# Kernel tuning notes

Measured on AMD Instinct MI355X. Metric: run time of the kernel, lower is better.

The kernel has to match this reference:

```python
import jax, jax.numpy as jnp
import numpy as np

CT1, CT2, ETA = 0.15, 0.1, 0.5
B, K, C = 65536, 50, 10


def setup_inputs() -> dict:
    key = jax.random.key(0)
    ks = jax.random.split(key, 8)
    # xavier_normal-ish scales for the small learned params
    att = jax.random.normal(ks[5], (C,), jnp.float32) * (np.sqrt(2.0) * np.sqrt(2.0 / (C + 1)))
    proj = jax.random.normal(ks[6], (C, C), jnp.float32) * (np.sqrt(2.0) * np.sqrt(2.0 / (C + C)))
    return {
        "anchors_weak": jax.random.normal(ks[0], (B, C), jnp.float32),
        "anchors_strong": jax.random.normal(ks[1], (B, C), jnp.float32),
        "anchors": jax.random.normal(ks[2], (B, C), jnp.float32),
        "neighbors": jax.random.normal(ks[3], (B, K, C), jnp.float32),
        "labels": jax.random.randint(ks[4], (B,), 0, C),
        "index": jnp.arange(B),
        "att": att,
        "proj_param": proj,
    }


def reference(anchors_weak, anchors_strong, anchors, neighbors, labels, index, att, proj_param):
    # confidence mask on weak-augmentation probabilities
    wap = jax.nn.softmax(anchors_weak, axis=1)              # [B,C]
    mask0 = jnp.max(wap, axis=1) > CT1
    idx0 = jnp.nonzero(mask0)[0]                            # data-dependent (eager)

    wap = wap[idx0]                                         # [b,C]
    nbp = jax.nn.softmax(neighbors, axis=2)[idx0]           # [b,K,C]
    ap = jax.nn.softmax(anchors, axis=1)[idx0]              # [b,C]
    a_strong = anchors_strong[idx0]                         # [b,C]
    img_f = anchors[idx0]                                   # [b,C]
    nb_f = neighbors[idx0]                                  # [b,K,C]
    b, c = wap.shape

    # einsum('kk,ijk->ijk', P, X) multiplies by diag(P)
    d = jnp.diagonal(proj_param)                            # [C]
    zi = img_f[:, None, :] * d                              # [b,K,C] (broadcast expand)
    zj = nb_f * d                                           # [b,K,C]
    zizj = zi * zj                                          # cross_product attention
    att_score = jax.nn.leaky_relu(jnp.einsum('k,bjk->bj', att, zizj))  # [b,K]
    att_val = jax.nn.softmax(att_score, axis=1)[..., None]  # [b,K,1]
    q_hat = jnp.sum(att_val * nbp, axis=1)                  # [b,C]

    beta = jnp.sum((ap - q_hat) ** 2, axis=1)               # [b] = ||.||^2
    k = max(int(ETA * b), 1)
    topk_min = -jax.lax.top_k(-beta, k)[0]                  # k smallest
    tau = topk_min[-1] / jnp.exp(jnp.asarray(-1.0))
    alpha = -jnp.log(beta / tau)                            # [b]

    qi = wap ** alpha[:, None]
    qi = qi / jnp.sum(qi, axis=1, keepdims=True)
    q = jnp.where((alpha > 1.0)[:, None], qi, wap)          # [b,C]

    max_prob = jnp.max(q, axis=1)
    target = jnp.argmax(q, axis=1)
    mask = max_prob > CT2
    idx1 = jnp.nonzero(mask)[0]
    target_masked = target[idx1]
    n = int(idx1.shape[0])

    # class balancing (torch.unique equivalent via fixed-size counts)
    counts = jax.ops.segment_sum(jnp.ones_like(target_masked, dtype=jnp.float32),
                                 target_masked, num_segments=c)
    freq = counts / n
    weight = jnp.where(counts > 0, 1.0 / jnp.log(1.02 + freq), 1.0)  # [C]

    inp = a_strong[idx1]                                    # [n,C]
    input_prob = jax.nn.log_softmax(inp, axis=1)
    q_mask = q[idx1]                                        # [n,C]
    w_avg = weight[None, :] / jnp.sum(weight) * jnp.mean(weight)
    loss = -jnp.sum(w_avg * q_mask * input_prob) / n

    return (loss, target_masked, labels[idx0][idx1], n)
```

## Files before the change

### kernel.cpp

```cpp
#include <hip/hip_runtime.h>
#include <math.h>

#define CC 10
#define KK 50

__global__ __launch_bounds__(256)
void kA(const float* __restrict__ aw, const float* __restrict__ an,
        const float* __restrict__ nbr, const float* __restrict__ att,
        const float* __restrict__ proj,
        float* __restrict__ wap, float* __restrict__ beta,
        int* __restrict__ flag0, int* __restrict__ hist, int B)
{
  int i = blockIdx.x * 256 + threadIdx.x;
  if (i >= B) return;

  float coef[CC];
#pragma unroll
  for (int c = 0; c < CC; ++c) { float d = proj[c * CC + c]; coef[c] = att[c] * d * d; }

  const float2* anp = reinterpret_cast<const float2*>(an + (size_t)i * CC);
  float av[CC];
#pragma unroll
  for (int c2 = 0; c2 < CC / 2; ++c2) { float2 t = anp[c2]; av[2*c2] = t.x; av[2*c2+1] = t.y; }
  float ci[CC];
#pragma unroll
  for (int c = 0; c < CC; ++c) ci[c] = coef[c] * av[c];

  const float2* rowp = reinterpret_cast<const float2*>(nbr + (size_t)i * (KK * CC));
  float den = 0.f;
  float qh[CC];
#pragma unroll
  for (int c = 0; c < CC; ++c) qh[c] = 0.f;

#pragma unroll 5
  for (int k = 0; k < KK; ++k) {
    float nb[CC];
#pragma unroll
    for (int c2 = 0; c2 < CC / 2; ++c2) {
      float2 t = rowp[k * (CC / 2) + c2];
      nb[2*c2] = t.x; nb[2*c2+1] = t.y;
    }
    float s = 0.f;
#pragma unroll
    for (int c = 0; c < CC; ++c) s = fmaf(ci[c], nb[c], s);
    s = (s > 0.f) ? s : 0.01f * s;
    float en[CC]; float sn = 0.f;
#pragma unroll
    for (int c = 0; c < CC; ++c) { en[c] = __expf(nb[c]); sn += en[c]; }
    float e = __expf(s);
    den += e;
    float esc = e * __builtin_amdgcn_rcpf(sn);
#pragma unroll
    for (int c = 0; c < CC; ++c) qh[c] = fmaf(esc, en[c], qh[c]);
  }
  float invd = __builtin_amdgcn_rcpf(den);

  float ap[CC]; float s2 = 0.f;
#pragma unroll
  for (int c = 0; c < CC; ++c) { ap[c] = __expf(av[c]); s2 += ap[c]; }
  float inv2 = __builtin_amdgcn_rcpf(s2);
  float dd = 0.f;
#pragma unroll
  for (int c = 0; c < CC; ++c) { float d1 = ap[c] * inv2 - qh[c] * invd; dd = fmaf(d1, d1, dd); }
  beta[i] = dd;

  const float2* awp = reinterpret_cast<const float2*>(aw + (size_t)i * CC);
  float wv[CC];
#pragma unroll
  for (int c2 = 0; c2 < CC / 2; ++c2) { float2 t = awp[c2]; wv[2*c2] = t.x; wv[2*c2+1] = t.y; }
  float ew[CC]; float sw = 0.f, mxw = 0.f;
#pragma unroll
  for (int c = 0; c < CC; ++c) { ew[c] = __expf(wv[c]); sw += ew[c]; mxw = fmaxf(mxw, ew[c]); }
  float rsw = __builtin_amdgcn_rcpf(sw);
  float2* wq = reinterpret_cast<float2*>(wap + (size_t)i * CC);
#pragma unroll
  for (int c2 = 0; c2 < CC / 2; ++c2) {
    float2 t; t.x = ew[2*c2] * rsw; t.y = ew[2*c2+1] * rsw; wq[c2] = t;
  }
  int f = (mxw * rsw > 0.15f) ? 1 : 0;
  flag0[i] = f;
  if (f) atomicAdd(&hist[__float_as_uint(dd) >> 16], 1);
}

__global__ __launch_bounds__(1024)
void k3b_sel(const int* __restrict__ hist, int* __restrict__ scal)
{
  __shared__ int tmp[1024];
  int t = threadIdx.x;
  int base = t * 64;
  const int4* h4 = reinterpret_cast<const int4*>(hist + base);
  int sum = 0;
#pragma unroll
  for (int jj = 0; jj < 16; ++jj) { int4 v = h4[jj]; sum += v.x + v.y + v.z + v.w; }
  tmp[t] = sum;
  __syncthreads();
  for (int off = 1; off < 1024; off <<= 1) {
    int v = (t >= off) ? tmp[t - off] : 0;
    __syncthreads();
    tmp[t] += v;
    __syncthreads();
  }
  int cumb = tmp[t] - sum;
  int b = tmp[1023];
  int k = (int)(0.5 * (double)b);
  if (k < 1) k = 1;
  if (t == 0) scal[4] = k;
  if (b > 0 && k > cumb && k <= cumb + sum) {
    int c = cumb;
    for (int jj = 0; jj < 64; ++jj) {
      int h = hist[base + jj];
      if (k <= c + h) { scal[2] = base + jj; scal[3] = k - c; break; }
      c += h;
    }
  }
  if (b == 0 && t == 0) { scal[2] = 0; scal[3] = 1; }
}

__global__ __launch_bounds__(256)
void k3c_hist2(const float* __restrict__ beta, const int* __restrict__ flag0,
               const int* __restrict__ scal, int* __restrict__ hist2, int B)
{
  int i = blockIdx.x * 256 + threadIdx.x;
  if (i >= B) return;
  if (flag0[i]) {
    unsigned key = __float_as_uint(beta[i]);
    if ((int)(key >> 16) == scal[2]) atomicAdd(&hist2[key & 0xFFFF], 1);
  }
}

__global__ __launch_bounds__(1024)
void k3d_tau(const int* __restrict__ hist2, int* __restrict__ scal,
             float* __restrict__ tau)
{
  __shared__ int tmp[1024];
  int t = threadIdx.x;
  int base = t * 64;
  const int4* h4 = reinterpret_cast<const int4*>(hist2 + base);
  int sum = 0;
#pragma unroll
  for (int jj = 0; jj < 16; ++jj) { int4 v = h4[jj]; sum += v.x + v.y + v.z + v.w; }
  tmp[t] = sum;
  __syncthreads();
  for (int off = 1; off < 1024; off <<= 1) {
    int v = (t >= off) ? tmp[t - off] : 0;
    __syncthreads();
    tmp[t] += v;
    __syncthreads();
  }
  int cumb = tmp[t] - sum;
  int k2 = scal[3];
  if (k2 > cumb && k2 <= cumb + sum) {
    int c = cumb;
    for (int jj = 0; jj < 64; ++jj) {
      int h = hist2[base + jj];
      if (k2 <= c + h) {
        unsigned key = (((unsigned)scal[2]) << 16) | (unsigned)(base + jj);
        float bk = __uint_as_float(key);
        *tau = bk / expf(-1.0f);
        break;
      }
      c += h;
    }
  }
}

__global__ __launch_bounds__(256)
void k4_q(const float* __restrict__ wap, const float* __restrict__ beta,
          const int* __restrict__ flag0, const float* __restrict__ tau_p,
          float* __restrict__ qbuf, int* __restrict__ target, int* __restrict__ flag1,
          int* __restrict__ counts, int* __restrict__ blockcnt, int B)
{
  __shared__ int lcnt[CC];
  if (threadIdx.x < CC) lcnt[threadIdx.x] = 0;
  __syncthreads();

  int i = blockIdx.x * 256 + threadIdx.x;
  int f = 0;
  if (i < B) {
    float tau = *tau_p;
    float w[CC];
    const float2* p = reinterpret_cast<const float2*>(wap + (size_t)i * CC);
#pragma unroll
    for (int c = 0; c < CC / 2; ++c) { float2 t = p[c]; w[2*c] = t.x; w[2*c+1] = t.y; }
    float alpha = -__logf(beta[i] / tau);
    float q[CC];
    if (alpha > 1.0f) {
      float s = 0.f;
#pragma unroll
      for (int c = 0; c < CC; ++c) { q[c] = __expf(alpha * __logf(w[c])); s += q[c]; }
#pragma unroll
      for (int c = 0; c < CC; ++c) q[c] = q[c] / s;
    } else {
#pragma unroll
      for (int c = 0; c < CC; ++c) q[c] = w[c];
    }
    float mp = q[0]; int tg = 0;
#pragma unroll
    for (int c = 1; c < CC; ++c) if (q[c] > mp) { mp = q[c]; tg = c; }
    f = (flag0[i] && (mp > 0.1f)) ? 1 : 0;
    float2* qo = reinterpret_cast<float2*>(qbuf + (size_t)i * CC);
#pragma unroll
    for (int c = 0; c < CC / 2; ++c) { float2 t; t.x = q[2*c]; t.y = q[2*c+1]; qo[c] = t; }
    target[i] = tg;
    flag1[i] = f;
    if (f) atomicAdd(&lcnt[tg], 1);
  }
  __shared__ int red[256];
  red[threadIdx.x] = f;
  __syncthreads();
  for (int off = 128; off; off >>= 1) {
    if (threadIdx.x < off) red[threadIdx.x] += red[threadIdx.x + off];
    __syncthreads();
  }
  if (threadIdx.x == 0) blockcnt[blockIdx.x] = red[0];
  if (threadIdx.x < CC) {
    int v = lcnt[threadIdx.x];
    if (v) atomicAdd(&counts[threadIdx.x], v);
  }
}

__global__ __launch_bounds__(256)
void k6_out(const int* __restrict__ flag1, const int* __restrict__ target,
            const int* __restrict__ labels, const int* __restrict__ blockcnt,
            const float* __restrict__ a_strong, const float* __restrict__ qbuf,
            const int* __restrict__ counts, float* __restrict__ out,
            float* __restrict__ lossp, int n_host, int nb, int B)
{
  __shared__ int tmp[256];
  __shared__ float wavg_s[CC];
  int t = threadIdx.x;

  int bv = (t < nb) ? blockcnt[t] : 0;
  tmp[t] = bv;
  __syncthreads();
  for (int off = 1; off < 256; off <<= 1) {
    int u = (t >= off) ? tmp[t - off] : 0;
    __syncthreads();
    tmp[t] += u;
    __syncthreads();
  }
  int n    = tmp[255];
  int boff = (blockIdx.x > 0) ? tmp[blockIdx.x - 1] : 0;
  if (t == 0) {
    float wt[CC]; float sumw = 0.f;
    for (int c = 0; c < CC; ++c) {
      int cnt = counts[c];
      float w_ = (cnt > 0) ? 1.0f / logf(1.02f + (float)cnt / (float)n) : 1.0f;
      wt[c] = w_; sumw += w_;
    }
    float meanw = sumw / (float)CC;
    for (int c = 0; c < CC; ++c) wavg_s[c] = wt[c] / sumw * meanw;
  }
  __syncthreads();

  int i = blockIdx.x * 256 + t;
  int f = (i < B) ? flag1[i] : 0;
  tmp[t] = f;
  __syncthreads();
  for (int off = 1; off < 256; off <<= 1) {
    int u = (t >= off) ? tmp[t - off] : 0;
    __syncthreads();
    tmp[t] += u;
    __syncthreads();
  }
  int pos = boff + tmp[t] - f;
  float part = 0.f;
  if (f) {
    out[1 + pos] = (float)target[i];
    out[1 + n_host + pos] = (float)labels[i];
    float x[CC];
    const float2* p = reinterpret_cast<const float2*>(a_strong + (size_t)i * CC);
#pragma unroll
    for (int c = 0; c < CC / 2; ++c) { float2 u2 = p[c]; x[2*c] = u2.x; x[2*c+1] = u2.y; }
    float m = x[0];
#pragma unroll
    for (int c = 1; c < CC; ++c) m = fmaxf(m, x[c]);
    float s = 0.f;
#pragma unroll
    for (int c = 0; c < CC; ++c) s += __expf(x[c] - m);
    float lse = m + __logf(s);
    const float2* qp = reinterpret_cast<const float2*>(qbuf + (size_t)i * CC);
    float q[CC];
#pragma unroll
    for (int c = 0; c < CC / 2; ++c) { float2 u2 = qp[c]; q[2*c] = u2.x; q[2*c+1] = u2.y; }
#pragma unroll
    for (int c = 0; c < CC; ++c) part += wavg_s[c] * q[c] * (x[c] - lse);
  }
  __shared__ float red[256];
  red[t] = part;
  __syncthreads();
  for (int off = 128; off; off >>= 1) {
    if (t < off) red[t] += red[t + off];
    __syncthreads();
  }
  if (t == 0) lossp[blockIdx.x] = red[0];
}

__global__ __launch_bounds__(256)
void k7_fin(const float* __restrict__ lossp, int nb, const int* __restrict__ blockcnt,
            float* __restrict__ out, int n_host)
{
  __shared__ float red[256];
  __shared__ int   redi[256];
  int t = threadIdx.x;
  float s = 0.f; int ns = 0;
  for (int jj = t; jj < nb; jj += 256) { s += lossp[jj]; ns += blockcnt[jj]; }
  red[t] = s; redi[t] = ns;
  __syncthreads();
  for (int off = 128; off; off >>= 1) {
    if (t < off) { red[t] += red[t + off]; redi[t] += redi[t + off]; }
    __syncthreads();
  }
  if (t == 0) {
    int n = redi[0];
    out[0] = -red[0] / (float)n;
    out[1 + 2 * n_host] = (float)n;
  }
}

extern "C" void kernel_launch(void* const* d_in, const int* in_sizes, int n_in,
                              void* d_out, int out_size, void* d_ws, size_t ws_size,
                              hipStream_t stream)
{
  const float* aw     = (const float*)d_in[0];
  const float* astr   = (const float*)d_in[1];
  const float* an     = (const float*)d_in[2];
  const float* nbr    = (const float*)d_in[3];
  const int*   labels = (const int*)d_in[4];
  const float* att    = (const float*)d_in[6];
  const float* proj   = (const float*)d_in[7];
  float* out = (float*)d_out;

  int B = in_sizes[4];
  int C = in_sizes[6];
  int K = (B > 0 && C > 0) ? in_sizes[3] / (B * C) : 0;
  if (C != CC || K != KK) return;
  int n_host = (out_size - 2) / 2;
  int nb = (B + 255) / 256;
  if (nb > 256) return;

  char* w = (char*)d_ws;
  size_t o = 0;
  auto alloc = [&](size_t bytes) { size_t r = o; o += (bytes + 255) & ~(size_t)255; return r; };
  size_t o_wap  = alloc((size_t)B * CC * 4);
  size_t o_q    = alloc((size_t)B * CC * 4);
  size_t o_beta = alloc((size_t)B * 4);
  size_t o_tgt  = alloc((size_t)B * 4);
  size_t o_f0   = alloc((size_t)B * 4);
  size_t o_f1   = alloc((size_t)B * 4);
  size_t o_bc   = alloc((size_t)nb * 4);
  size_t o_lp   = alloc((size_t)nb * 4);
  size_t zstart = o;
  size_t o_h1   = alloc(65536 * 4);
  size_t o_h2   = alloc(65536 * 4);
  size_t o_cnt  = alloc(64);
  size_t o_scal = alloc(64);
  size_t ztotal = o - zstart;
  if (o > ws_size) return;

  float* wap   = (float*)(w + o_wap);
  float* qbuf  = (float*)(w + o_q);
  float* beta  = (float*)(w + o_beta);
  int*   tgt   = (int*)(w + o_tgt);
  int*   f0    = (int*)(w + o_f0);
  int*   f1    = (int*)(w + o_f1);
  int*   bcnt  = (int*)(w + o_bc);
  float* lossp = (float*)(w + o_lp);
  int*   h1    = (int*)(w + o_h1);
  int*   h2    = (int*)(w + o_h2);
  int*   cnts  = (int*)(w + o_cnt);
  int*   scal  = (int*)(w + o_scal);
  float* taup  = (float*)(scal + 8);

  hipMemsetAsync(w + zstart, 0, ztotal, stream);

  kA      <<<nb, 256, 0, stream>>>(aw, an, nbr, att, proj, wap, beta, f0, h1, B);
  k3b_sel <<<1, 1024, 0, stream>>>(h1, scal);
  k3c_hist2<<<nb, 256, 0, stream>>>(beta, f0, scal, h2, B);
  k3d_tau <<<1, 1024, 0, stream>>>(h2, scal, taup);
  k4_q    <<<nb, 256, 0, stream>>>(wap, beta, f0, taup, qbuf, tgt, f1,
                                   cnts, bcnt, B);
  k6_out  <<<nb, 256, 0, stream>>>(f1, tgt, labels, bcnt, astr, qbuf, cnts,
                                   out, lossp, n_host, nb, B);
  k7_fin  <<<1, 256, 0, stream>>>(lossp, nb, bcnt, out, n_host);
}
```

Baseline: 102.2 us.

## Split neighbor loop across four lanes per row with shuffle reduction

The main kernel now gives each row to four threads instead of one. Each lane handles 12 or 13 of the 50 neighbors, and the partial softmax denominators and q_hat accumulators are combined with xor shuffles. Lane 0 alone writes beta, wap, the flag and the histogram entry. This is meant to raise parallelism and memory-level concurrency on the 128MB neighbor read. In exchange, every lane redundantly recomputes the anchor and weak softmax, and each row pays for the shuffle reductions.

New measurement: 133.0 us. 1.3x slower.

```diff
diff --git a/kernel.cpp b/kernel.cpp
--- a/kernel.cpp
+++ b/kernel.cpp
@@ -11,14 +11,16 @@
         float* __restrict__ wap, float* __restrict__ beta,
         int* __restrict__ flag0, int* __restrict__ hist, int B)
 {
-  int i = blockIdx.x * 256 + threadIdx.x;
-  if (i >= B) return;
+  int gt  = blockIdx.x * 256 + threadIdx.x;
+  int row = gt >> 2;
+  int j   = gt & 3;
+  if (row >= B) return;
 
   float coef[CC];
 #pragma unroll
   for (int c = 0; c < CC; ++c) { float d = proj[c * CC + c]; coef[c] = att[c] * d * d; }
 
-  const float2* anp = reinterpret_cast<const float2*>(an + (size_t)i * CC);
+  const float2* anp = reinterpret_cast<const float2*>(an + (size_t)row * CC);
   float av[CC];
 #pragma unroll
   for (int c2 = 0; c2 < CC / 2; ++c2) { float2 t = anp[c2]; av[2*c2] = t.x; av[2*c2+1] = t.y; }
@@ -26,19 +28,21 @@
 #pragma unroll
   for (int c = 0; c < CC; ++c) ci[c] = coef[c] * av[c];
 
-  const float2* rowp = reinterpret_cast<const float2*>(nbr + (size_t)i * (KK * CC));
+  const float2* rowp = reinterpret_cast<const float2*>(nbr + (size_t)row * (KK * CC));
   float den = 0.f;
   float qh[CC];
 #pragma unroll
   for (int c = 0; c < CC; ++c) qh[c] = 0.f;
 
-#pragma unroll 5
-  for (int k = 0; k < KK; ++k) {
+  int ks = j * 12;
+#pragma unroll 4
+  for (int t = 0; t < 12; ++t) {
+    int k = ks + t;
     float nb[CC];
 #pragma unroll
     for (int c2 = 0; c2 < CC / 2; ++c2) {
-      float2 t = rowp[k * (CC / 2) + c2];
-      nb[2*c2] = t.x; nb[2*c2+1] = t.y;
+      float2 v = rowp[k * (CC / 2) + c2];
+      nb[2*c2] = v.x; nb[2*c2+1] = v.y;
     }
     float s = 0.f;
 #pragma unroll
@@ -53,6 +57,34 @@
 #pragma unroll
     for (int c = 0; c < CC; ++c) qh[c] = fmaf(esc, en[c], qh[c]);
   }
+  if (j < 2) {
+    int k = 48 + j;
+    float nb[CC];
+#pragma unroll
+    for (int c2 = 0; c2 < CC / 2; ++c2) {
+      float2 v = rowp[k * (CC / 2) + c2];
+      nb[2*c2] = v.x; nb[2*c2+1] = v.y;
+    }
+    float s = 0.f;
+#pragma unroll
+    for (int c = 0; c < CC; ++c) s = fmaf(ci[c], nb[c], s);
+    s = (s > 0.f) ? s : 0.01f * s;
+    float en[CC]; float sn = 0.f;
+#pragma unroll
+    for (int c = 0; c < CC; ++c) { en[c] = __expf(nb[c]); sn += en[c]; }
+    float e = __expf(s);
+    den += e;
+    float esc = e * __builtin_amdgcn_rcpf(sn);
+#pragma unroll
+    for (int c = 0; c < CC; ++c) qh[c] = fmaf(esc, en[c], qh[c]);
+  }
+
+#pragma unroll
+  for (int off = 1; off <= 2; off <<= 1) {
+    den += __shfl_xor(den, off);
+#pragma unroll
+    for (int c = 0; c < CC; ++c) qh[c] += __shfl_xor(qh[c], off);
+  }
   float invd = __builtin_amdgcn_rcpf(den);
 
   float ap[CC]; float s2 = 0.f;
@@ -62,9 +94,8 @@
   float dd = 0.f;
 #pragma unroll
   for (int c = 0; c < CC; ++c) { float d1 = ap[c] * inv2 - qh[c] * invd; dd = fmaf(d1, d1, dd); }
-  beta[i] = dd;
-
-  const float2* awp = reinterpret_cast<const float2*>(aw + (size_t)i * CC);
+
+  const float2* awp = reinterpret_cast<const float2*>(aw + (size_t)row * CC);
   float wv[CC];
 #pragma unroll
   for (int c2 = 0; c2 < CC / 2; ++c2) { float2 t = awp[c2]; wv[2*c2] = t.x; wv[2*c2+1] = t.y; }
@@ -72,14 +103,18 @@
 #pragma unroll
   for (int c = 0; c < CC; ++c) { ew[c] = __expf(wv[c]); sw += ew[c]; mxw = fmaxf(mxw, ew[c]); }
   float rsw = __builtin_amdgcn_rcpf(sw);
-  float2* wq = reinterpret_cast<float2*>(wap + (size_t)i * CC);
-#pragma unroll
-  for (int c2 = 0; c2 < CC / 2; ++c2) {
-    float2 t; t.x = ew[2*c2] * rsw; t.y = ew[2*c2+1] * rsw; wq[c2] = t;
-  }
-  int f = (mxw * rsw > 0.15f) ? 1 : 0;
-  flag0[i] = f;
-  if (f) atomicAdd(&hist[__float_as_uint(dd) >> 16], 1);
+
+  if (j == 0) {
+    beta[row] = dd;
+    float2* wq = reinterpret_cast<float2*>(wap + (size_t)row * CC);
+#pragma unroll
+    for (int c2 = 0; c2 < CC / 2; ++c2) {
+      float2 t; t.x = ew[2*c2] * rsw; t.y = ew[2*c2+1] * rsw; wq[c2] = t;
+    }
+    int f = (mxw * rsw > 0.15f) ? 1 : 0;
+    flag0[row] = f;
+    if (f) atomicAdd(&hist[__float_as_uint(dd) >> 16], 1);
+  }
 }
 
 __global__ __launch_bounds__(1024)
@@ -374,7 +409,8 @@
 
   hipMemsetAsync(w + zstart, 0, ztotal, stream);
 
-  kA      <<<nb, 256, 0, stream>>>(aw, an, nbr, att, proj, wap, beta, f0, h1, B);
+  int nbA = (B * 4 + 255) / 256;
+  kA      <<<nbA, 256, 0, stream>>>(aw, an, nbr, att, proj, wap, beta, f0, h1, B);
   k3b_sel <<<1, 1024, 0, stream>>>(h1, scal);
   k3c_hist2<<<nb, 256, 0, stream>>>(beta, f0, scal, h2, B);
   k3d_tau <<<1, 1024, 0, stream>>>(h2, scal, taup);
```

## Split neighbor loop of kA across four waves with shared-memory reduction

Applied to the files above, without the earlier changes.

Each block now handles 64 rows instead of 256, with its four waves each processing a quarter of the 50 neighbors for the same row. Partial softmax-attention sums (den and qh) go through shared memory and are combined by wave 0, which then finishes the per-row work. This shortens the serial per-thread chain and raises parallelism (4x more threads), meant to improve latency hiding on the memory-bound neighbor read. In exchange it adds a __syncthreads, shared-memory traffic, and leaves three waves idle during the epilogue. Per-lane memory access stays strided by row (2000 bytes apart), so coalescing is unchanged.

After: 107.3 us. 1.05x slower.

```diff
diff --git a/kernel.cpp b/kernel.cpp
--- a/kernel.cpp
+++ b/kernel.cpp
@@ -11,14 +11,20 @@
         float* __restrict__ wap, float* __restrict__ beta,
         int* __restrict__ flag0, int* __restrict__ hist, int B)
 {
-  int i = blockIdx.x * 256 + threadIdx.x;
-  if (i >= B) return;
+  __shared__ float part[3][64][13];
+
+  int tid  = threadIdx.x;
+  int wave = tid >> 6;
+  int lane = tid & 63;
+  int row  = blockIdx.x * 64 + lane;
+  bool valid = (row < B);
+  int lrow = valid ? row : 0;
 
   float coef[CC];
 #pragma unroll
   for (int c = 0; c < CC; ++c) { float d = proj[c * CC + c]; coef[c] = att[c] * d * d; }
 
-  const float2* anp = reinterpret_cast<const float2*>(an + (size_t)i * CC);
+  const float2* anp = reinterpret_cast<const float2*>(an + (size_t)lrow * CC);
   float av[CC];
 #pragma unroll
   for (int c2 = 0; c2 < CC / 2; ++c2) { float2 t = anp[c2]; av[2*c2] = t.x; av[2*c2+1] = t.y; }
@@ -26,19 +32,24 @@
 #pragma unroll
   for (int c = 0; c < CC; ++c) ci[c] = coef[c] * av[c];
 
-  const float2* rowp = reinterpret_cast<const float2*>(nbr + (size_t)i * (KK * CC));
   float den = 0.f;
   float qh[CC];
 #pragma unroll
   for (int c = 0; c < CC; ++c) qh[c] = 0.f;
 
-#pragma unroll 5
-  for (int k = 0; k < KK; ++k) {
+  int ks = (wave == 0) ? 0 : (wave == 1) ? 13 : (wave == 2) ? 26 : 38;
+  int kc = (wave < 2) ? 13 : 12;
+  const float2* rowp = reinterpret_cast<const float2*>(nbr + (size_t)lrow * (KK * CC))
+                       + ks * (CC / 2);
+
+#pragma unroll 4
+  for (int t = 0; t < 13; ++t) {
+    if (t >= kc) break;
     float nb[CC];
 #pragma unroll
     for (int c2 = 0; c2 < CC / 2; ++c2) {
-      float2 t = rowp[k * (CC / 2) + c2];
-      nb[2*c2] = t.x; nb[2*c2+1] = t.y;
+      float2 v = rowp[t * (CC / 2) + c2];
+      nb[2*c2] = v.x; nb[2*c2+1] = v.y;
     }
     float s = 0.f;
 #pragma unroll
@@ -53,6 +64,22 @@
 #pragma unroll
     for (int c = 0; c < CC; ++c) qh[c] = fmaf(esc, en[c], qh[c]);
   }
+
+  if (wave > 0) {
+    part[wave - 1][lane][0] = den;
+#pragma unroll
+    for (int c = 0; c < CC; ++c) part[wave - 1][lane][1 + c] = qh[c];
+  }
+  __syncthreads();
+  if (wave != 0) return;
+
+#pragma unroll
+  for (int w = 0; w < 3; ++w) {
+    den += part[w][lane][0];
+#pragma unroll
+    for (int c = 0; c < CC; ++c) qh[c] += part[w][lane][1 + c];
+  }
+  if (!valid) return;
   float invd = __builtin_amdgcn_rcpf(den);
 
   float ap[CC]; float s2 = 0.f;
@@ -62,9 +89,9 @@
   float dd = 0.f;
 #pragma unroll
   for (int c = 0; c < CC; ++c) { float d1 = ap[c] * inv2 - qh[c] * invd; dd = fmaf(d1, d1, dd); }
-  beta[i] = dd;
-
-  const float2* awp = reinterpret_cast<const float2*>(aw + (size_t)i * CC);
+  beta[row] = dd;
+
+  const float2* awp = reinterpret_cast<const float2*>(aw + (size_t)row * CC);
   float wv[CC];
 #pragma unroll
   for (int c2 = 0; c2 < CC / 2; ++c2) { float2 t = awp[c2]; wv[2*c2] = t.x; wv[2*c2+1] = t.y; }
@@ -72,13 +99,13 @@
 #pragma unroll
   for (int c = 0; c < CC; ++c) { ew[c] = __expf(wv[c]); sw += ew[c]; mxw = fmaxf(mxw, ew[c]); }
   float rsw = __builtin_amdgcn_rcpf(sw);
-  float2* wq = reinterpret_cast<float2*>(wap + (size_t)i * CC);
+  float2* wq = reinterpret_cast<float2*>(wap + (size_t)row * CC);
 #pragma unroll
   for (int c2 = 0; c2 < CC / 2; ++c2) {
     float2 t; t.x = ew[2*c2] * rsw; t.y = ew[2*c2+1] * rsw; wq[c2] = t;
   }
   int f = (mxw * rsw > 0.15f) ? 1 : 0;
-  flag0[i] = f;
+  flag0[row] = f;
   if (f) atomicAdd(&hist[__float_as_uint(dd) >> 16], 1);
 }
 
@@ -374,7 +401,8 @@
 
   hipMemsetAsync(w + zstart, 0, ztotal, stream);
 
-  kA      <<<nb, 256, 0, stream>>>(aw, an, nbr, att, proj, wap, beta, f0, h1, B);
+  int nbA = (B + 63) / 64;
+  kA      <<<nbA, 256, 0, stream>>>(aw, an, nbr, att, proj, wap, beta, f0, h1, B);
   k3b_sel <<<1, 1024, 0, stream>>>(h1, scal);
   k3c_hist2<<<nb, 256, 0, stream>>>(beta, f0, scal, h2, B);
   k3d_tau <<<1, 1024, 0, stream>>>(h2, scal, taup);
```
